# Performance work log

Measured on AMD Instinct MI355X. Metric: run time of the kernel, lower is better.

The kernel has to match this reference:

```python
import jax, jax.numpy as jnp
import numpy as np

WIN = 21            # window_pixel_wh
SIGMA = 2.0
B, H, W, C = 16, 1008, 1008, 1
HS, WS = H // WIN, W // WIN      # 48, 48 window grid
T = HS * WS                      # num_tracks = 2304
P = WIN * WIN                    # 441 pixels per window


def _build_constants():
    # Window-center positions mapped to logical coords in [-1, 1]
    xs, ys = np.meshgrid(np.arange(WS, dtype=np.float32) * WIN,
                         np.arange(HS, dtype=np.float32) * WIN)
    px = xs + WIN // 2
    py = ys + WIN // 2
    win_pos = np.stack([2.0 * px / W - 1.0, 2.0 * py / H - 1.0], axis=-1)
    win_pos = win_pos.reshape(1, T, 1, 2).astype(np.float32)
    # Gaussian window weights: exp(-r^2 / (2 sigma^2)) over pixel radius.
    c = WIN // 2
    yy, xx = np.mgrid[0:WIN, 0:WIN]
    r2 = ((xx - c) ** 2 + (yy - c) ** 2).astype(np.float32)
    weights = np.exp(-r2 / (2.0 * SIGMA ** 2)).reshape(1, 1, P, 1).astype(np.float32)
    center_rel = np.array([W / WIN, H / WIN], dtype=np.float32).reshape(1, 1, 1, 2)
    sx = np.array([[-3, 0, 3], [-10, 0, 10], [-3, 0, 3]], np.float32).reshape(3, 3, 1, 1)
    sy = np.array([[-3, -10, -3], [0, 0, 0], [3, 10, 3]], np.float32).reshape(3, 3, 1, 1)
    return (jnp.asarray(win_pos), jnp.asarray(weights), jnp.asarray(center_rel),
            jnp.asarray(sx), jnp.asarray(sy))

WIN_POS, WEIGHTS, CENTER_REL, SCHARR_X, SCHARR_Y = _build_constants()


def _split_windows(img):
    o = img[:, :HS * WIN, :WS * WIN]
    o = o.reshape(-1, HS, WIN, WS, WIN, C)
    return o.transpose(0, 1, 3, 2, 4, 5).reshape(-1, T, WIN, WIN, C)


def setup_inputs() -> dict:
    key = jax.random.key(0)
    imgs = jax.random.uniform(key, (B, 2, H, W, C), dtype=jnp.float32)
    return {"imgs": imgs}


def reference(imgs):
    ff = imgs[:, 0]   # first frame  [B,H,W,C]
    sf = imgs[:, 1]   # second frame
    dn = ('NHWC', 'HWIO', 'NHWC')
    ff_dx = jax.lax.conv_general_dilated(ff, SCHARR_X, (1, 1), 'SAME', dimension_numbers=dn)
    ff_dy = jax.lax.conv_general_dilated(ff, SCHARR_Y, (1, 1), 'SAME', dimension_numbers=dn)

    ffw = _split_windows(ff)
    sfw = _split_windows(sf)
    Ix = _split_windows(ff_dx).reshape(-1, T, P, 1)
    Iy = _split_windows(ff_dy).reshape(-1, T, P, 1)

    A = jnp.concatenate([Ix, Iy], axis=3)          # [B,T,P,2]
    ATA = jnp.einsum('btpi,btpj->btij', A, A * WEIGHTS)  # [B,T,2,2]
    a = ATA[..., 0, 0]; b = ATA[..., 0, 1]
    c = ATA[..., 1, 0]; d = ATA[..., 1, 1]
    det = a * d - b * c
    inv_det = jnp.where(det != 0.0, 1.0 / jnp.where(det != 0.0, det, 1.0), 0.0)  # divide_no_nan
    # tf: stack([stack([d,-b],-1), stack([-c,a],-1)], axis=3)
    ATA_inv = inv_det[..., None, None] * jnp.stack(
        [jnp.stack([d, -b], axis=-1), jnp.stack([-c, a], axis=-1)], axis=3)

    rhs = -(sfw - ffw).reshape(-1, T, P, 1) * WEIGHTS   # [B,T,P,1]
    ATb = jnp.einsum('btpi,btpk->btik', A, rhs)          # [B,T,2,1]
    VxVy = ATA_inv @ ATb                                 # [B,T,2,1]

    vels = VxVy.transpose(0, 1, 3, 2)                    # [B,T,1,2]
    vels = vels / CENTER_REL + WIN_POS
    wp = jnp.broadcast_to(WIN_POS, vels.shape)
    return jnp.concatenate([wp, vels], axis=2)           # [B,T,2,2]
```

## Files before the change

### kernel.cpp

```cpp
#include <hip/hip_runtime.h>


constexpr int HH   = 1008;
constexpr int WW   = 1008;
constexpr int WINN = 21;
constexpr int HSN  = 48;
constexpr int WSN  = 48;
constexpr int TN   = HSN * WSN;
constexpr int SEGS = 4;
constexpr int COLS = WW / SEGS;
constexpr int WPB  = WSN / SEGS;

__global__ __launch_bounds__(256)
void SparseOptFlowLK_kernel(const float* __restrict__ imgs,
                            float* __restrict__ out) {
    const int bi  = blockIdx.x;
    const int b   = bi / (HSN * SEGS);
    const int rem = bi % (HSN * SEGS);
    const int hy  = rem / SEGS;
    const int seg = rem % SEGS;

    const float* __restrict__ ff = imgs + (size_t)b * (2ull * HH * WW);
    const float* __restrict__ sf = ff + (size_t)HH * WW;

    __shared__ float colsum[5][COLS];
    __shared__ float red[WPB][5];

    const int lx = threadIdx.x;

    if (lx < COLS) {
        const int gx = seg * COLS + lx;
        const bool hl = (gx > 0);
        const bool hr = (gx < WW - 1);

        float wtab[WINN];
        #pragma unroll
        for (int y = 0; y < WINN; ++y) {
            const float dy = (float)(y - 10);
            wtab[y] = expf(-dy * dy * 0.125f);
        }
        const int   xw  = lx % WINN;
        const float wxw = wtab[xw];

        const int g0 = hy * WINN;

        float rm0, rm1, rm2, rc0, rc1, rc2;
        if (g0 > 0) {
            const float* r = ff + (size_t)(g0 - 1) * WW;
            rm1 = r[gx];
            rm0 = hl ? r[gx - 1] : 0.0f;
            rm2 = hr ? r[gx + 1] : 0.0f;
        } else {
            rm0 = rm1 = rm2 = 0.0f;
        }
        {
            const float* r = ff + (size_t)g0 * WW;
            rc1 = r[gx];
            rc0 = hl ? r[gx - 1] : 0.0f;
            rc2 = hr ? r[gx + 1] : 0.0f;
        }

        float sA = 0.0f, sB = 0.0f, sD = 0.0f, sX = 0.0f, sY = 0.0f;

        #pragma unroll
        for (int y = 0; y < WINN; ++y) {
            float rp0, rp1, rp2;
            const int gp = g0 + y + 1;
            if (gp < HH) {
                const float* r = ff + (size_t)gp * WW;
                rp1 = r[gx];
                rp0 = hl ? r[gx - 1] : 0.0f;
                rp2 = hr ? r[gx + 1] : 0.0f;
            } else {
                rp0 = rp1 = rp2 = 0.0f;
            }

            const float Ix = 3.0f * (rm2 - rm0) + 10.0f * (rc2 - rc0) + 3.0f * (rp2 - rp0);
            const float Iy = 3.0f * (rp0 - rm0) + 10.0f * (rp1 - rm1) + 3.0f * (rp2 - rm2);

            const float df = rc1 - sf[(size_t)(g0 + y) * WW + gx];
            const float w  = wxw * wtab[y];

            sA += w * Ix * Ix;
            sB += w * Ix * Iy;
            sD += w * Iy * Iy;
            sX += w * Ix * df;
            sY += w * Iy * df;

            rm0 = rc0; rm1 = rc1; rm2 = rc2;
            rc0 = rp0; rc1 = rp1; rc2 = rp2;
        }

        colsum[0][lx] = sA;
        colsum[1][lx] = sB;
        colsum[2][lx] = sD;
        colsum[3][lx] = sX;
        colsum[4][lx] = sY;
    }
    __syncthreads();

    if (lx < WPB * 5) {
        const int w = lx / 5;
        const int s = lx % 5;
        float sum = 0.0f;
        #pragma unroll
        for (int j = 0; j < WINN; ++j) sum += colsum[s][w * WINN + j];
        red[w][s] = sum;
    }
    __syncthreads();

    if (lx < WPB) {
        const float A  = red[lx][0];
        const float Bv = red[lx][1];
        const float D  = red[lx][2];
        const float Bx = red[lx][3];
        const float By = red[lx][4];

        const float det = A * D - Bv * Bv;
        const float inv = (det != 0.0f) ? (1.0f / det) : 0.0f;
        const float vx  = inv * ( D * Bx - Bv * By);
        const float vy  = inv * (-Bv * Bx + A  * By);

        const int wxg = seg * WPB + lx;
        const float wpx = 2.0f * (float)(wxg * WINN + WINN / 2) / (float)WW - 1.0f;
        const float wpy = 2.0f * (float)(hy  * WINN + WINN / 2) / (float)HH - 1.0f;

        const int t = hy * WSN + wxg;
        float4 o;
        o.x = wpx;
        o.y = wpy;
        o.z = vx / 48.0f + wpx;
        o.w = vy / 48.0f + wpy;
        reinterpret_cast<float4*>(out)[(size_t)b * TN + t] = o;
    }
}

extern "C" void kernel_launch(void* const* d_in, const int* in_sizes, int n_in,
                              void* d_out, int out_size, void* d_ws, size_t ws_size,
                              hipStream_t stream) {
    const float* imgs = (const float*)d_in[0];
    float* out = (float*)d_out;

    const int B = in_sizes[0] / (2 * HH * WW);
    const dim3 grid(B * HSN * SEGS);
    SparseOptFlowLK_kernel<<<grid, 256, 0, stream>>>(imgs, out);
}
```

Baseline: 182.4 us.

## Process a full window row per block with float4 loads and wave shuffles for halos

Each block now covers a whole row of windows (1008 columns) instead of a quarter. Each lane loads four adjacent columns with float4 loads and gets its left and right neighbours through wave shuffles, so the per-column scalar loads of three neighbours go away. Row weights move to a constant table and column weights use fast exp. The grid shrinks fourfold, so there is less parallelism, but each thread does more work with vectorised memory access.

```diff
diff --git a/kernel.cpp b/kernel.cpp
--- a/kernel.cpp
+++ b/kernel.cpp
@@ -7,109 +7,131 @@
 constexpr int HSN  = 48;
 constexpr int WSN  = 48;
 constexpr int TN   = HSN * WSN;
-constexpr int SEGS = 4;
-constexpr int COLS = WW / SEGS;
-constexpr int WPB  = WSN / SEGS;
+
+__device__ __constant__ const float kWY[WINN] = {
+    3.7266532e-6f, 4.0065297e-5f, 3.3546262e-4f, 2.1874911e-3f,
+    1.1108997e-2f, 4.3936934e-2f, 1.3533528e-1f, 3.2465247e-1f,
+    6.0653066e-1f, 8.8249690e-1f, 1.0f,          8.8249690e-1f,
+    6.0653066e-1f, 3.2465247e-1f, 1.3533528e-1f, 4.3936934e-2f,
+    1.1108997e-2f, 2.1874911e-3f, 3.3546262e-4f, 4.0065297e-5f,
+    3.7266532e-6f };
+
+struct Row { float4 v; float l, r; };
+
+__device__ __forceinline__ Row zero_row() {
+    Row z; z.v = make_float4(0.f, 0.f, 0.f, 0.f); z.l = 0.f; z.r = 0.f;
+    return z;
+}
+
+__device__ __forceinline__ Row load_row(const float* __restrict__ rp,
+                                        int c0, int ln, bool act) {
+    Row r;
+    float4 v = make_float4(0.f, 0.f, 0.f, 0.f);
+    if (act) v = *reinterpret_cast<const float4*>(rp + c0);
+    r.v = v;
+    r.l = __shfl_up(v.w, 1);
+    r.r = __shfl_down(v.x, 1);
+    if (ln == 0)  r.l = (c0 > 0)       ? rp[c0 - 1] : 0.0f;
+    if (ln == 62) r.r = (c0 + 4 < WW)  ? rp[c0 + 4] : 0.0f;
+    return r;
+}
 
 __global__ __launch_bounds__(256)
 void SparseOptFlowLK_kernel(const float* __restrict__ imgs,
                             float* __restrict__ out) {
-    const int bi  = blockIdx.x;
-    const int b   = bi / (HSN * SEGS);
-    const int rem = bi % (HSN * SEGS);
-    const int hy  = rem / SEGS;
-    const int seg = rem % SEGS;
+    const int bi = blockIdx.x;
+    const int b  = bi / HSN;
+    const int hy = bi % HSN;
 
     const float* __restrict__ ff = imgs + (size_t)b * (2ull * HH * WW);
     const float* __restrict__ sf = ff + (size_t)HH * WW;
 
-    __shared__ float colsum[5][COLS];
-    __shared__ float red[WPB][5];
+    __shared__ float4 colsum4[5][WW / 4];
+    __shared__ float  red[WSN][5];
 
-    const int lx = threadIdx.x;
+    const int  lx  = threadIdx.x;
+    const int  wv  = lx >> 6;
+    const int  ln  = lx & 63;
+    const bool act = (ln < 63);
+    const int  c0  = wv * 252 + 4 * ln;
 
-    if (lx < COLS) {
-        const int gx = seg * COLS + lx;
-        const bool hl = (gx > 0);
-        const bool hr = (gx < WW - 1);
+    const int g0 = hy * WINN;
 
-        float wtab[WINN];
+    float wx[4];
+    {
+        int m = c0 % WINN;
         #pragma unroll
-        for (int y = 0; y < WINN; ++y) {
-            const float dy = (float)(y - 10);
-            wtab[y] = expf(-dy * dy * 0.125f);
+        for (int c = 0; c < 4; ++c) {
+            int mc = m + c; if (mc >= WINN) mc -= WINN;
+            const float dx = (float)(mc - 10);
+            wx[c] = __expf(-dx * dx * 0.125f);
         }
-        const int   xw  = lx % WINN;
-        const float wxw = wtab[xw];
+    }
 
-        const int g0 = hy * WINN;
+    Row rt = (g0 > 0) ? load_row(ff + (size_t)(g0 - 1) * WW, c0, ln, act)
+                      : zero_row();
+    Row rm = load_row(ff + (size_t)g0 * WW, c0, ln, act);
 
-        float rm0, rm1, rm2, rc0, rc1, rc2;
-        if (g0 > 0) {
-            const float* r = ff + (size_t)(g0 - 1) * WW;
-            rm1 = r[gx];
-            rm0 = hl ? r[gx - 1] : 0.0f;
-            rm2 = hr ? r[gx + 1] : 0.0f;
-        } else {
-            rm0 = rm1 = rm2 = 0.0f;
-        }
-        {
-            const float* r = ff + (size_t)g0 * WW;
-            rc1 = r[gx];
-            rc0 = hl ? r[gx - 1] : 0.0f;
-            rc2 = hr ? r[gx + 1] : 0.0f;
-        }
+    float sA[4] = {0,0,0,0}, sB[4] = {0,0,0,0}, sD[4] = {0,0,0,0};
+    float sX[4] = {0,0,0,0}, sY[4] = {0,0,0,0};
 
-        float sA = 0.0f, sB = 0.0f, sD = 0.0f, sX = 0.0f, sY = 0.0f;
+    #pragma unroll
+    for (int y = 0; y < WINN; ++y) {
+        const int gp = g0 + y + 1;
+        Row rb = (gp < HH) ? load_row(ff + (size_t)gp * WW, c0, ln, act)
+                           : zero_row();
+        float4 sfv = make_float4(0.f, 0.f, 0.f, 0.f);
+        if (act) sfv = *reinterpret_cast<const float4*>(
+                           sf + (size_t)(g0 + y) * WW + c0);
+
+        const float wy = kWY[y];
+
+        const float T[6] = { rt.l, rt.v.x, rt.v.y, rt.v.z, rt.v.w, rt.r };
+        const float M[6] = { rm.l, rm.v.x, rm.v.y, rm.v.z, rm.v.w, rm.r };
+        const float Bo[6] = { rb.l, rb.v.x, rb.v.y, rb.v.z, rb.v.w, rb.r };
+        const float SF[4] = { sfv.x, sfv.y, sfv.z, sfv.w };
 
         #pragma unroll
-        for (int y = 0; y < WINN; ++y) {
-            float rp0, rp1, rp2;
-            const int gp = g0 + y + 1;
-            if (gp < HH) {
-                const float* r = ff + (size_t)gp * WW;
-                rp1 = r[gx];
-                rp0 = hl ? r[gx - 1] : 0.0f;
-                rp2 = hr ? r[gx + 1] : 0.0f;
-            } else {
-                rp0 = rp1 = rp2 = 0.0f;
-            }
+        for (int c = 0; c < 4; ++c) {
+            const float Ix = 3.0f * (T[c+2] - T[c]) + 10.0f * (M[c+2] - M[c])
+                           + 3.0f * (Bo[c+2] - Bo[c]);
+            const float Iy = 3.0f * (Bo[c] - T[c]) + 10.0f * (Bo[c+1] - T[c+1])
+                           + 3.0f * (Bo[c+2] - T[c+2]);
+            const float df = M[c+1] - SF[c];
+            const float w  = wx[c] * wy;
+            const float wIx = w * Ix, wIy = w * Iy;
+            sA[c] += wIx * Ix;
+            sB[c] += wIx * Iy;
+            sD[c] += wIy * Iy;
+            sX[c] += wIx * df;
+            sY[c] += wIy * df;
+        }
+        rt = rm; rm = rb;
+    }
 
-            const float Ix = 3.0f * (rm2 - rm0) + 10.0f * (rc2 - rc0) + 3.0f * (rp2 - rp0);
-            const float Iy = 3.0f * (rp0 - rm0) + 10.0f * (rp1 - rm1) + 3.0f * (rp2 - rm2);
-
-            const float df = rc1 - sf[(size_t)(g0 + y) * WW + gx];
-            const float w  = wxw * wtab[y];
-
-            sA += w * Ix * Ix;
-            sB += w * Ix * Iy;
-            sD += w * Iy * Iy;
-            sX += w * Ix * df;
-            sY += w * Iy * df;
-
-            rm0 = rc0; rm1 = rc1; rm2 = rc2;
-            rc0 = rp0; rc1 = rp1; rc2 = rp2;
-        }
-
-        colsum[0][lx] = sA;
-        colsum[1][lx] = sB;
-        colsum[2][lx] = sD;
-        colsum[3][lx] = sX;
-        colsum[4][lx] = sY;
+    if (act) {
+        const int ci = wv * 63 + ln;
+        colsum4[0][ci] = make_float4(sA[0], sA[1], sA[2], sA[3]);
+        colsum4[1][ci] = make_float4(sB[0], sB[1], sB[2], sB[3]);
+        colsum4[2][ci] = make_float4(sD[0], sD[1], sD[2], sD[3]);
+        colsum4[3][ci] = make_float4(sX[0], sX[1], sX[2], sX[3]);
+        colsum4[4][ci] = make_float4(sY[0], sY[1], sY[2], sY[3]);
     }
     __syncthreads();
 
-    if (lx < WPB * 5) {
+    if (lx < WSN * 5) {
         const int w = lx / 5;
         const int s = lx % 5;
+        const float* cs = reinterpret_cast<const float*>(colsum4)
+                        + s * WW + w * WINN;
         float sum = 0.0f;
         #pragma unroll
-        for (int j = 0; j < WINN; ++j) sum += colsum[s][w * WINN + j];
+        for (int j = 0; j < WINN; ++j) sum += cs[j];
         red[w][s] = sum;
     }
     __syncthreads();
 
-    if (lx < WPB) {
+    if (lx < WSN) {
         const float A  = red[lx][0];
         const float Bv = red[lx][1];
         const float D  = red[lx][2];
@@ -121,17 +143,15 @@
         const float vx  = inv * ( D * Bx - Bv * By);
         const float vy  = inv * (-Bv * Bx + A  * By);
 
-        const int wxg = seg * WPB + lx;
-        const float wpx = 2.0f * (float)(wxg * WINN + WINN / 2) / (float)WW - 1.0f;
-        const float wpy = 2.0f * (float)(hy  * WINN + WINN / 2) / (float)HH - 1.0f;
+        const float wpx = 2.0f * (float)(lx * WINN + WINN / 2) / (float)WW - 1.0f;
+        const float wpy = 2.0f * (float)(hy * WINN + WINN / 2) / (float)HH - 1.0f;
 
-        const int t = hy * WSN + wxg;
         float4 o;
         o.x = wpx;
         o.y = wpy;
         o.z = vx / 48.0f + wpx;
         o.w = vy / 48.0f + wpy;
-        reinterpret_cast<float4*>(out)[(size_t)b * TN + t] = o;
+        reinterpret_cast<float4*>(out)[(size_t)b * TN + hy * WSN + lx] = o;
     }
 }
 
@@ -142,6 +162,6 @@
     float* out = (float*)d_out;
 
     const int B = in_sizes[0] / (2 * HH * WW);
-    const dim3 grid(B * HSN * SEGS);
+    const dim3 grid(B * HSN);
     SparseOptFlowLK_kernel<<<grid, 256, 0, stream>>>(imgs, out);
 }
```

Result: slower. 203.6 us (+11.6%).
